# Optimization experiments

Hardware: AMD Instinct MI355X
Metric: run time of the kernel (lower is better)

The kernel has to match this reference:

```python
import jax, jax.numpy as jnp
import numpy as np

B, NPG, DEG = 512, 128, 16          # graphs, nodes/graph, out-degree
N = B * NPG                          # 65536 nodes
E = N * DEG                          # 1048576 edges
IN_DIM, HID, HEADS = 11, 32, 4
K1 = int(np.ceil(0.8 * NPG))         # 103 nodes/graph after pool1
K2 = int(np.ceil(0.8 * K1))          # 83 nodes/graph after pool2


def gat_conv(x, src, dst, mask, W, a_s, a_d, b, n_nodes):
    # PyG GATConv (concat=True, add_self_loops=True, eval mode -> no dropout)
    xp = (x @ W).reshape(n_nodes, HEADS, HID)            # [N,H,C]
    as_ = jnp.einsum('nhc,hc->nh', xp, a_s)
    ad_ = jnp.einsum('nhc,hc->nh', xp, a_d)
    loop = jnp.arange(n_nodes)
    s = jnp.concatenate([src, loop])
    d = jnp.concatenate([dst, loop])
    m = jnp.concatenate([mask, jnp.ones(n_nodes, bool)])
    logit = jax.nn.leaky_relu(as_[s] + ad_[d], 0.2)      # [E+N,H]
    logit = jnp.where(m[:, None], logit, -1e9)
    mx = jax.ops.segment_max(logit, d, num_segments=n_nodes)
    ex = jnp.exp(logit - mx[d]) * m[:, None]
    den = jax.ops.segment_sum(ex, d, num_segments=n_nodes)
    alpha = ex / (den[d] + 1e-16)                        # segment softmax over dst
    out = jax.ops.segment_sum(alpha[:, :, None] * xp[s], d, num_segments=n_nodes)
    return out.reshape(n_nodes, HEADS * HID) + b


def topk_pool(x, src, dst, mask, w, npg, k):
    # PyG TopKPooling: score = tanh((x*w).sum(-1)/||w||); keep top ceil(ratio*n) per graph
    nb = x.shape[0] // npg
    score = jnp.tanh((x @ w) / jnp.linalg.norm(w))
    vals, idx = jax.lax.top_k(score.reshape(nb, npg), k)  # [B,k]
    perm = (idx + (jnp.arange(nb) * npg)[:, None]).reshape(-1)
    x_new = x[perm] * vals.reshape(-1, 1)
    remap = jnp.full(nb * npg, -1).at[perm].set(jnp.arange(nb * k))
    ns, nd = remap[src], remap[dst]
    m = mask & (ns >= 0) & (nd >= 0)
    return x_new, jnp.where(m, ns, 0), jnp.where(m, nd, 0), m


def setup_inputs():
    key = jax.random.key(0)
    ks = jax.random.split(key, 24)
    s = 0.05
    x = jax.random.normal(ks[0], (N, IN_DIM), jnp.float32)
    src = jnp.repeat(jnp.arange(N), DEG)
    dst = (src // NPG) * NPG + jax.random.randint(ks[1], (E,), 0, NPG)
    edge_index = jnp.stack([src, dst])
    edge_attr = jax.random.normal(ks[2], (E, 4), jnp.float32)
    batch = jnp.repeat(jnp.arange(B), NPG)
    p = dict(
        W_g1=jax.random.normal(ks[3], (IN_DIM, HEADS * HID), jnp.float32) * s,
        att_src1=jax.random.normal(ks[4], (HEADS, HID), jnp.float32) * s,
        att_dst1=jax.random.normal(ks[5], (HEADS, HID), jnp.float32) * s,
        b_g1=jnp.zeros((HEADS * HID,), jnp.float32),
        W_t1=jax.random.normal(ks[6], (HEADS * HID, HID), jnp.float32) * s,
        b_t1=jnp.zeros((HID,), jnp.float32),
        pool_w1=jax.random.normal(ks[7], (HID,), jnp.float32) * s,
        W_g2=jax.random.normal(ks[8], (HID, HEADS * HID), jnp.float32) * s,
        att_src2=jax.random.normal(ks[9], (HEADS, HID), jnp.float32) * s,
        att_dst2=jax.random.normal(ks[10], (HEADS, HID), jnp.float32) * s,
        b_g2=jnp.zeros((HEADS * HID,), jnp.float32),
        W_t2=jax.random.normal(ks[11], (HEADS * HID, HID), jnp.float32) * s,
        b_t2=jnp.zeros((HID,), jnp.float32),
        pool_w2=jax.random.normal(ks[12], (HID,), jnp.float32) * s,
        W_l1=jax.random.normal(ks[13], (2 * HID, 256), jnp.float32) * s,
        b_l1=jnp.zeros((256,), jnp.float32),
        W_l2=jax.random.normal(ks[14], (256, 1024), jnp.float32) * s,
        b_l2=jnp.zeros((1024,), jnp.float32),
        W_l3=jax.random.normal(ks[15], (1024, 1), jnp.float32) * s,
        b_l3=jnp.zeros((1,), jnp.float32),
    )
    return dict(x=x, edge_index=edge_index, edge_attr=edge_attr, batch=batch, **p)


def reference(x, edge_index, edge_attr, batch,
              W_g1, att_src1, att_dst1, b_g1, W_t1, b_t1, pool_w1,
              W_g2, att_src2, att_dst2, b_g2, W_t2, b_t2, pool_w2,
              W_l1, b_l1, W_l2, b_l2, W_l3, b_l3):
    # edge_attr is ignored (GATConv built without edge_dim); batch is implicit
    # in the fixed equal-size graph layout.  Eval mode -> dropout disabled.
    src, dst = edge_index[0], edge_index[1]
    mask = jnp.ones(E, bool)
    h = jax.nn.relu(gat_conv(x, src, dst, mask, W_g1, att_src1, att_dst1, b_g1, N))
    h = h @ W_t1 + b_t1
    h, src, dst, mask = topk_pool(h, src, dst, mask, pool_w1, NPG, K1)
    h1 = h.reshape(B, K1, HID)
    g1 = jnp.concatenate([h1.max(1), h1.mean(1)], axis=1)   # [B, 2*HID]
    h = jax.nn.relu(gat_conv(h, src, dst, mask, W_g2, att_src2, att_dst2, b_g2, B * K1))
    h = h @ W_t2 + b_t2
    h, src, dst, mask = topk_pool(h, src, dst, mask, pool_w2, K1, K2)
    h2 = h.reshape(B, K2, HID)
    g2 = jnp.concatenate([h2.max(1), h2.mean(1)], axis=1)
    g = g1 + g2
    g = jax.nn.relu(g @ W_l1 + b_l1)
    g = jax.nn.relu(g @ W_l2 + b_l2)
    return g @ W_l3 + b_l3                                   # [B,1]
```

## Files before the change

kernel.cpp:

```cpp
#include <hip/hip_runtime.h>
#include <math.h>

constexpr int NPGc  = 128;
constexpr int NG    = 512;
constexpr int EPGc  = 2048;
constexpr int ETOT  = 1048576;
constexpr int IND   = 11;
constexpr int HIDc  = 32;
constexpr int FD    = 128;
constexpr int K1c   = 103;
constexpr int K2c   = 83;
constexpr int NN    = NG * NPGc;
constexpr int N2c   = NG * K1c;
constexpr int EPAD  = 2432;
constexpr int SBCAP = 2560;
constexpr int OFFSTR= 264;

__device__ __forceinline__ float lrelu(float x){ return fmaxf(x, 0.2f*x); }

__device__ __forceinline__ void agg4(const float4* __restrict__ X4, int r, int cbase, float e,
                                     float4& A0, float4& A1, float4& A2, float4& A3)
{
    int b = r * 8, s = r & 7;
    float4 u0 = X4[b + ((cbase+0) ^ s)];
    A0.x = fmaf(e, u0.x, A0.x); A0.y = fmaf(e, u0.y, A0.y); A0.z = fmaf(e, u0.z, A0.z); A0.w = fmaf(e, u0.w, A0.w);
    float4 u1 = X4[b + ((cbase+1) ^ s)];
    A1.x = fmaf(e, u1.x, A1.x); A1.y = fmaf(e, u1.y, A1.y); A1.z = fmaf(e, u1.z, A1.z); A1.w = fmaf(e, u1.w, A1.w);
    float4 u2 = X4[b + ((cbase+2) ^ s)];
    A2.x = fmaf(e, u2.x, A2.x); A2.y = fmaf(e, u2.y, A2.y); A2.z = fmaf(e, u2.z, A2.z); A2.w = fmaf(e, u2.w, A2.w);
    float4 u3 = X4[b + ((cbase+3) ^ s)];
    A3.x = fmaf(e, u3.x, A3.x); A3.y = fmaf(e, u3.y, A3.y); A3.z = fmaf(e, u3.z, A3.z); A3.w = fmaf(e, u3.w, A3.w);
}

template<int KIN>
__device__ void foldDev(const float* __restrict__ Wg, const float* __restrict__ avs,
                        const float* __restrict__ avd, float* __restrict__ S, float* __restrict__ D, int t)
{
    if (t < KIN * 4) {
        int k = t >> 2, h = t & 3;
        float s = 0.f, d = 0.f;
        for (int j = 0; j < HIDc; j++) {
            float w = Wg[k*FD + h*HIDc + j];
            s = fmaf(w, avs[h*HIDc + j], s);
            d = fmaf(w, avd[h*HIDc + j], d);
        }
        S[t] = s; D[t] = d;
    }
}

__global__ __launch_bounds__(256) void k_prep(const int* __restrict__ ei,
    const float* __restrict__ W1g, const float* __restrict__ s1, const float* __restrict__ d1,
    const float* __restrict__ W2g, const float* __restrict__ s2, const float* __restrict__ d2,
    int* __restrict__ csrOff, unsigned char* __restrict__ csrSB,
    float* __restrict__ S1, float* __restrict__ D1, float* __restrict__ S2, float* __restrict__ D2)
{
    int b = blockIdx.x, t = threadIdx.x;
    if (b >= NG) {
        if (b == NG)     foldDev<IND>(W1g, s1, d1, S1, D1, t);
        else             foldDev<HIDc>(W2g, s2, d2, S2, D2, t);
        return;
    }
    int g = b;
    __shared__ int cnt[128], cur[128], offL[129];
    __shared__ __align__(16) unsigned char sbL[SBCAP];
    const int FILL1 = (int)0x80808080u;
    if (t < 128) cnt[t] = 0;
    if (t < SBCAP/16) ((int4*)sbL)[t] = make_int4(FILL1, FILL1, FILL1, FILL1);
    __syncthreads();
    const int* dstG = ei + ETOT + g * EPGc;
    int dnv[8];
    #pragma unroll
    for (int q = 0; q < 8; q++) {
        int e = t + 256*q;
        dnv[q] = dstG[e] - g * NPGc;
        atomicAdd(&cnt[dnv[q]], 1);
    }
    __syncthreads();
    if (t < 64) {
        int c0 = cnt[2*t], c1 = cnt[2*t + 1];
        int p0 = (c0 + 3) & ~3, p1 = (c1 + 3) & ~3;
        int ps = p0 + p1, P = ps;
        #pragma unroll
        for (int dl = 1; dl < 64; dl <<= 1) { int v = __shfl_up(P, dl); if (t >= dl) P += v; }
        int E0 = P - ps;
        offL[2*t] = E0; offL[2*t + 1] = E0 + p0;
        cur[2*t]  = E0; cur[2*t + 1]  = E0 + p0;
        if (t == 63) offL[128] = P;
    }
    __syncthreads();
    #pragma unroll
    for (int q = 0; q < 8; q++) {
        int e = t + 256*q;
        int pos = atomicAdd(&cur[dnv[q]], 1);
        sbL[pos] = (unsigned char)(e >> 4);
    }
    __syncthreads();
    if (t < SBCAP/16) ((int4*)(csrSB + (size_t)g * SBCAP))[t] = ((const int4*)sbL)[t];
    if (t <= 128) csrOff[g*OFFSTR + t] = offL[t];
    if (t < 128)  csrOff[g*OFFSTR + 132 + t] = cur[t];
}

template<int NNODE, int KIN>
__global__ __launch_bounds__(256) void k_gat(
    const float* __restrict__ xin, const float* __restrict__ Wg,
    const float* __restrict__ WsS, const float* __restrict__ WsD,
    const int* __restrict__ csrOff, const unsigned char* __restrict__ csrSB,
    const float* __restrict__ bias, const float* __restrict__ Wt,
    float* __restrict__ htp)
{
    int g = blockIdx.x, h = blockIdx.y, t = threadIdx.x;
    __shared__ __align__(16) float xpL[NNODE * 32];
    __shared__ __align__(16) float WL[KIN * 32];
    __shared__ __align__(16) unsigned char sbL[SBCAP];
    __shared__ float asL[NNODE + 1], adL[NNODE];
    __shared__ unsigned short offL[NNODE + 1];

    const float* xg = xin + (size_t)g * NNODE * KIN;

    for (int i = t; i < KIN * 32; i += 256) { int k = i >> 5, c = i & 31; WL[i] = Wg[k*FD + h*32 + c]; }
    if (t <= NNODE) offL[t] = (unsigned short)csrOff[g*OFFSTR + t];
    if (t < SBCAP/16) ((int4*)sbL)[t] = ((const int4*)(csrSB + (size_t)g * SBCAP))[t];
    if (t == 0) asL[NNODE] = -1e30f;
    __syncthreads();

    for (int p = t; p < NNODE * 8; p += 256) {
        int n = p >> 3, c4 = p & 7;
        float4 acc = make_float4(0.f, 0.f, 0.f, 0.f);
        if constexpr ((KIN & 3) == 0) {
            const float4* xr4 = (const float4*)(xg + (size_t)n * KIN);
            #pragma unroll
            for (int k4 = 0; k4 < KIN/4; k4++) {
                float4 xv = xr4[k4];
                float4 w;
                w = *(const float4*)&WL[(k4*4+0)*32 + c4*4];
                acc.x = fmaf(xv.x, w.x, acc.x); acc.y = fmaf(xv.x, w.y, acc.y); acc.z = fmaf(xv.x, w.z, acc.z); acc.w = fmaf(xv.x, w.w, acc.w);
                w = *(const float4*)&WL[(k4*4+1)*32 + c4*4];
                acc.x = fmaf(xv.y, w.x, acc.x); acc.y = fmaf(xv.y, w.y, acc.y); acc.z = fmaf(xv.y, w.z, acc.z); acc.w = fmaf(xv.y, w.w, acc.w);
                w = *(const float4*)&WL[(k4*4+2)*32 + c4*4];
                acc.x = fmaf(xv.z, w.x, acc.x); acc.y = fmaf(xv.z, w.y, acc.y); acc.z = fmaf(xv.z, w.z, acc.z); acc.w = fmaf(xv.z, w.w, acc.w);
                w = *(const float4*)&WL[(k4*4+3)*32 + c4*4];
                acc.x = fmaf(xv.w, w.x, acc.x); acc.y = fmaf(xv.w, w.y, acc.y); acc.z = fmaf(xv.w, w.z, acc.z); acc.w = fmaf(xv.w, w.w, acc.w);
            }
        } else {
            const float* xr = xg + (size_t)n * KIN;
            #pragma unroll
            for (int k = 0; k < KIN; k++) {
                float xv = xr[k];
                float4 w4 = *(const float4*)&WL[k*32 + c4*4];
                acc.x = fmaf(xv, w4.x, acc.x); acc.y = fmaf(xv, w4.y, acc.y);
                acc.z = fmaf(xv, w4.z, acc.z); acc.w = fmaf(xv, w4.w, acc.w);
            }
        }
        ((float4*)xpL)[n*8 + (c4 ^ (n & 7))] = acc;
    }
    if (t < NNODE) {
        const float* xr = xg + (size_t)t * KIN;
        float s = 0.f, d = 0.f;
        #pragma unroll
        for (int k = 0; k < KIN; k++) { float v = xr[k]; s = fmaf(v, WsS[k*4 + h], s); d = fmaf(v, WsD[k*4 + h], d); }
        asL[t] = s; adL[t] = d;
    }
    __syncthreads();

    const float4* X4 = (const float4*)xpL;
    float4 A0, A1, A2, A3;
    int n = 0, cbase = 0;
    bool act = (t < NNODE * 2);
    if (act) {
        n = t >> 1;
        const int half = t & 1;
        cbase = half * 4;
        float as_n = asL[n], adn = adL[n];
        int lo = offL[n], hi = offL[n + 1];
        int mid = lo + (((hi - lo) >> 3) << 2);
        int slo = half ? mid : lo;
        int shi = half ? hi  : mid;
        float mx = -INFINITY;
        for (int i = slo; i < shi; i += 4) {
            unsigned int q4 = *(const unsigned int*)(sbL + i);
            float a0 = asL[q4 & 255], a1 = asL[(q4 >> 8) & 255];
            float a2 = asL[(q4 >> 16) & 255], a3 = asL[q4 >> 24];
            mx = fmaxf(fmaxf(fmaxf(fmaxf(mx, a0), a1), a2), a3);
        }
        mx = fmaxf(mx, __shfl_xor(mx, 1));
        mx = fmaxf(mx, as_n);
        float m = lrelu(mx + adn);
        float den = half ? 0.f : expf(lrelu(as_n + adn) - m);
        for (int i = slo; i < shi; i += 4) {
            unsigned int q4 = *(const unsigned int*)(sbL + i);
            den += expf(lrelu(asL[q4 & 255] + adn) - m);
            den += expf(lrelu(asL[(q4 >> 8) & 255] + adn) - m);
            den += expf(lrelu(asL[(q4 >> 16) & 255] + adn) - m);
            den += expf(lrelu(asL[q4 >> 24] + adn) - m);
        }
        den += __shfl_xor(den, 1);
        float inv = 1.f / (den + 1e-16f);
        float w0 = expf(lrelu(as_n + adn) - m);
        int sw = n & 7, nb = n * 8;
        float4 v0 = X4[nb + ((cbase+0) ^ sw)];
        A0 = make_float4(w0*v0.x, w0*v0.y, w0*v0.z, w0*v0.w);
        float4 v1 = X4[nb + ((cbase+1) ^ sw)];
        A1 = make_float4(w0*v1.x, w0*v1.y, w0*v1.z, w0*v1.w);
        float4 v2 = X4[nb + ((cbase+2) ^ sw)];
        A2 = make_float4(w0*v2.x, w0*v2.y, w0*v2.z, w0*v2.w);
        float4 v3 = X4[nb + ((cbase+3) ^ sw)];
        A3 = make_float4(w0*v3.x, w0*v3.y, w0*v3.z, w0*v3.w);
        for (int s = lo; s < hi; s += 4) {
            unsigned int q4 = *(const unsigned int*)(sbL + s);
            int s0 = q4 & 255, s1 = (q4 >> 8) & 255, s2 = (q4 >> 16) & 255, s3 = q4 >> 24;
            float e0 = expf(lrelu(asL[s0] + adn) - m);
            float e1 = expf(lrelu(asL[s1] + adn) - m);
            float e2 = expf(lrelu(asL[s2] + adn) - m);
            float e3 = expf(lrelu(asL[s3] + adn) - m);
            agg4(X4, min(s0, NNODE-1), cbase, e0, A0, A1, A2, A3);
            agg4(X4, min(s1, NNODE-1), cbase, e1, A0, A1, A2, A3);
            agg4(X4, min(s2, NNODE-1), cbase, e2, A0, A1, A2, A3);
            agg4(X4, min(s3, NNODE-1), cbase, e3, A0, A1, A2, A3);
        }
        const float* bb = bias + h*32 + cbase*4;
        float4 b0 = *(const float4*)(bb);
        float4 b1 = *(const float4*)(bb + 4);
        float4 b2 = *(const float4*)(bb + 8);
        float4 b3 = *(const float4*)(bb + 12);
        A0.x = fmaxf(fmaf(A0.x, inv, b0.x), 0.f); A0.y = fmaxf(fmaf(A0.y, inv, b0.y), 0.f);
        A0.z = fmaxf(fmaf(A0.z, inv, b0.z), 0.f); A0.w = fmaxf(fmaf(A0.w, inv, b0.w), 0.f);
        A1.x = fmaxf(fmaf(A1.x, inv, b1.x), 0.f); A1.y = fmaxf(fmaf(A1.y, inv, b1.y), 0.f);
        A1.z = fmaxf(fmaf(A1.z, inv, b1.z), 0.f); A1.w = fmaxf(fmaf(A1.w, inv, b1.w), 0.f);
        A2.x = fmaxf(fmaf(A2.x, inv, b2.x), 0.f); A2.y = fmaxf(fmaf(A2.y, inv, b2.y), 0.f);
        A2.z = fmaxf(fmaf(A2.z, inv, b2.z), 0.f); A2.w = fmaxf(fmaf(A2.w, inv, b2.w), 0.f);
        A3.x = fmaxf(fmaf(A3.x, inv, b3.x), 0.f); A3.y = fmaxf(fmaf(A3.y, inv, b3.y), 0.f);
        A3.z = fmaxf(fmaf(A3.z, inv, b3.z), 0.f); A3.w = fmaxf(fmaf(A3.w, inv, b3.w), 0.f);
    }
    __syncthreads();
    if (act) {
        float4* X4w = (float4*)xpL;
        int sw = n & 7, nb = n * 8;
        X4w[nb + ((cbase+0) ^ sw)] = A0;
        X4w[nb + ((cbase+1) ^ sw)] = A1;
        X4w[nb + ((cbase+2) ^ sw)] = A2;
        X4w[nb + ((cbase+3) ^ sw)] = A3;
    }
    __syncthreads();

    {
        const int n0 = t >> 3, j4 = t & 7;
        const float* WtH = Wt + h*1024 + j4*4;
        #pragma unroll
        for (int rr = 0; rr < 4; rr++) {
            int nn = n0 + rr*32;
            if (nn < NNODE) {
                float4 acc = make_float4(0.f, 0.f, 0.f, 0.f);
                int sw = nn & 7, nb = nn * 8;
                #pragma unroll
                for (int c4 = 0; c4 < 8; c4++) {
                    float4 xv = X4[nb + (c4 ^ sw)];
                    float4 w;
                    w = *(const float4*)(WtH + (c4*4+0)*32);
                    acc.x = fmaf(xv.x, w.x, acc.x); acc.y = fmaf(xv.x, w.y, acc.y); acc.z = fmaf(xv.x, w.z, acc.z); acc.w = fmaf(xv.x, w.w, acc.w);
                    w = *(const float4*)(WtH + (c4*4+1)*32);
                    acc.x = fmaf(xv.y, w.x, acc.x); acc.y = fmaf(xv.y, w.y, acc.y); acc.z = fmaf(xv.y, w.z, acc.z); acc.w = fmaf(xv.y, w.w, acc.w);
                    w = *(const float4*)(WtH + (c4*4+2)*32);
                    acc.x = fmaf(xv.z, w.x, acc.x); acc.y = fmaf(xv.z, w.y, acc.y); acc.z = fmaf(xv.z, w.z, acc.z); acc.w = fmaf(xv.z, w.w, acc.w);
                    w = *(const float4*)(WtH + (c4*4+3)*32);
                    acc.x = fmaf(xv.w, w.x, acc.x); acc.y = fmaf(xv.w, w.y, acc.y); acc.z = fmaf(xv.w, w.z, acc.z); acc.w = fmaf(xv.w, w.w, acc.w);
                }
                *(float4*)(htp + ((size_t)(g * NNODE + nn) * 4 + h) * 32 + j4 * 4) = acc;
            }
        }
    }
}

template<int NIN, int KEEP, bool FIRST>
__global__ __launch_bounds__(512) void k_linpool(
    const float* __restrict__ htp, const float* __restrict__ bt, const float* __restrict__ pw,
    float* __restrict__ xnew, const int* __restrict__ ei,
    int* __restrict__ csrOffW, unsigned char* __restrict__ sbW,
    float* __restrict__ gfeat, const float* __restrict__ gprev,
    const float* __restrict__ W1, const float* __restrict__ b1,
    const float* __restrict__ W2, const float* __restrict__ b2,
    const float* __restrict__ W3, const float* __restrict__ b3,
    float* __restrict__ outp)
{
    int g = blockIdx.x, t = threadIdx.x;
    __shared__ float htL[NIN * 33];
    __shared__ float scoreL[NIN];
    __shared__ int rnkL[NIN];
    __shared__ int cnt[128], cur[128], offL[129];
    __shared__ __align__(16) unsigned char sbL[SBCAP];
    __shared__ float gvec[64];
    __shared__ float h1L[256], red[512];

    for (int p = t; p < NIN * 8; p += 512) {
        int n = p >> 3, q = p & 7;
        const float4* row = (const float4*)(htp + (size_t)(g * NIN + n) * 128);
        float4 s = ((const float4*)bt)[q];
        float4 p0 = row[q], p1 = row[8 + q], p2 = row[16 + q], p3 = row[24 + q];
        s.x += p0.x; s.y += p0.y; s.z += p0.z; s.w += p0.w;
        s.x += p1.x; s.y += p1.y; s.z += p1.z; s.w += p1.w;
        s.x += p2.x; s.y += p2.y; s.z += p2.z; s.w += p2.w;
        s.x += p3.x; s.y += p3.y; s.z += p3.z; s.w += p3.w;
        float* d = htL + n*33 + q*4;
        d[0] = s.x; d[1] = s.y; d[2] = s.z; d[3] = s.w;
    }
    __syncthreads();

    float nrm; { float ss = 0.f; for (int k = 0; k < HIDc; k++) { float w = pw[k]; ss = fmaf(w, w, ss); } nrm = sqrtf(ss); }
    if (t < NIN) {
        float dot = 0.f;
        #pragma unroll
        for (int k = 0; k < HIDc; k++) dot = fmaf(htL[t*33 + k], pw[k], dot);
        scoreL[t] = tanhf(dot / nrm);
    }
    __syncthreads();
    if (t < NIN) {
        float si = scoreL[t]; int rank = 0;
        #pragma unroll 8
        for (int q = 0; q < NIN; q++) {
            float sj = scoreL[q];
            rank += (sj > si || (sj == si && q < t)) ? 1 : 0;
        }
        rnkL[t] = (rank < KEEP) ? rank : -1;
    }
    __syncthreads();
    if constexpr (FIRST) {
        for (int p = t; p < NIN * 32; p += 512) {
            int n = p >> 5, jj = p & 31;
            int rk = rnkL[n];
            if (rk >= 0) xnew[((size_t)g*KEEP + rk)*HIDc + jj] = htL[n*33 + jj] * scoreL[n];
        }
    }
    if (t < HIDc) {
        float mx = -INFINITY, sm = 0.f;
        #pragma unroll 4
        for (int n = 0; n < NIN; n++) {
            if (rnkL[n] >= 0) { float v = htL[n*33 + t] * scoreL[n]; mx = fmaxf(mx, v); sm += v; }
        }
        float mean = sm / (float)KEEP;
        if constexpr (FIRST) {
            gfeat[(size_t)g*64 + t]      = mx;
            gfeat[(size_t)g*64 + 32 + t] = mean;
        } else {
            gvec[t]      = gprev[(size_t)g*64 + t] + mx;
            gvec[32 + t] = gprev[(size_t)g*64 + 32 + t] + mean;
        }
    }

    if constexpr (FIRST) {
        __syncthreads();
        const int FILL2 = (int)0x67676767u;
        if (t < 128) cnt[t] = 0;
        if (t < SBCAP/16) ((int4*)sbL)[t] = make_int4(FILL2, FILL2, FILL2, FILL2);
        __syncthreads();
        const int* dstG = ei + ETOT + g * EPGc;
        int snv[4], dnv[4];
        #pragma unroll
        for (int q = 0; q < 4; q++) {
            int e = t + 512*q;
            int s = rnkL[e >> 4], d = rnkL[dstG[e] - g * NPGc];
            bool ok = (s >= 0 && d >= 0);
            snv[q] = s; dnv[q] = ok ? d : -1;
            if (ok) atomicAdd(&cnt[d], 1);
        }
        __syncthreads();
        if (t < 64) {
            int c0 = cnt[2*t], c1 = cnt[2*t + 1];
            int p0 = (c0 + 3) & ~3, p1 = (c1 + 3) & ~3;
            int ps = p0 + p1, P = ps;
            #pragma unroll
            for (int dl = 1; dl < 64; dl <<= 1) { int v = __shfl_up(P, dl); if (t >= dl) P += v; }
            int E0 = P - ps;
            offL[2*t] = E0; offL[2*t + 1] = E0 + p0;
            cur[2*t]  = E0; cur[2*t + 1]  = E0 + p0;
            if (t == 63) offL[128] = P;
        }
        __syncthreads();
        #pragma unroll
        for (int q = 0; q < 4; q++) {
            if (dnv[q] >= 0) {
                int pos = atomicAdd(&cur[dnv[q]], 1);
                sbL[pos] = (unsigned char)snv[q];
            }
        }
        __syncthreads();
        if (t < SBCAP/16) ((int4*)(sbW + (size_t)g * SBCAP))[t] = ((const int4*)sbL)[t];
        if (t <= K1c) csrOffW[g*OFFSTR + t] = offL[t];
        if (t < K1c)  csrOffW[g*OFFSTR + 132 + t] = cur[t];
    } else {
        __syncthreads();
        if (t < 256) {
            float a = b1[t];
            #pragma unroll 8
            for (int k = 0; k < 64; k++) a = fmaf(gvec[k], W1[k*256 + t], a);
            h1L[t] = fmaxf(a, 0.f);
        }
        __syncthreads();
        float2 bq = *(const float2*)(b2 + 2*t);
        float c0 = bq.x, c1 = bq.y;
        const float2* w2r = (const float2*)W2 + t;
        #pragma unroll 8
        for (int i = 0; i < 256; i++) {
            float hv = h1L[i];
            float2 w = w2r[(size_t)i * 512];
            c0 = fmaf(hv, w.x, c0);
            c1 = fmaf(hv, w.y, c1);
        }
        float2 w3q = *(const float2*)(W3 + 2*t);
        float p = fmaf(fmaxf(c0, 0.f), w3q.x, fmaxf(c1, 0.f) * w3q.y);
        red[t] = p;
        __syncthreads();
        for (int s = 256; s > 0; s >>= 1) { if (t < s) red[t] += red[t + s]; __syncthreads(); }
        if (t == 0) outp[g] = red[0] + b3[0];
    }
}

extern "C" void kernel_launch(void* const* d_in, const int* in_sizes, int n_in,
                              void* d_out, int out_size, void* d_ws, size_t ws_size,
                              hipStream_t stream)
{
    const float* x    = (const float*)d_in[0];
    const int*   ei   = (const int*)  d_in[1];
    const float* W_g1 = (const float*)d_in[4];
    const float* as1w = (const float*)d_in[5];
    const float* ad1w = (const float*)d_in[6];
    const float* b_g1 = (const float*)d_in[7];
    const float* W_t1 = (const float*)d_in[8];
    const float* b_t1 = (const float*)d_in[9];
    const float* pw1  = (const float*)d_in[10];
    const float* W_g2 = (const float*)d_in[11];
    const float* as2w = (const float*)d_in[12];
    const float* ad2w = (const float*)d_in[13];
    const float* b_g2 = (const float*)d_in[14];
    const float* W_t2 = (const float*)d_in[15];
    const float* b_t2 = (const float*)d_in[16];
    const float* pw2  = (const float*)d_in[17];
    const float* W_l1 = (const float*)d_in[18];
    const float* b_l1 = (const float*)d_in[19];
    const float* W_l2 = (const float*)d_in[20];
    const float* b_l2 = (const float*)d_in[21];
    const float* W_l3 = (const float*)d_in[22];
    const float* b_l3 = (const float*)d_in[23];
    float* out = (float*)d_out;

    char* ws = (char*)d_ws;
    size_t off = 0;
    auto alloc = [&](size_t bytes) -> void* {
        void* p = (void*)(ws + off);
        off += ((bytes + 255) / 256) * 256;
        return p;
    };
    float* htp1  = (float*)alloc((size_t)NN * 128 * 4);
    float* htp2  = (float*)alloc((size_t)N2c * 128 * 4);
    float* x2    = (float*)alloc((size_t)N2c * HIDc * 4);
    float* g1    = (float*)alloc((size_t)NG * 64 * 4);
    float* wsS1  = (float*)alloc(64 * 4);
    float* wsD1  = (float*)alloc(64 * 4);
    float* wsS2  = (float*)alloc(128 * 4);
    float* wsD2  = (float*)alloc(128 * 4);
    int*   off1  = (int*)  alloc((size_t)NG * OFFSTR * 4);
    unsigned char* sb1 = (unsigned char*)alloc((size_t)NG * SBCAP);
    int*   off2  = (int*)  alloc((size_t)NG * OFFSTR * 4);
    unsigned char* sb2 = (unsigned char*)alloc((size_t)NG * SBCAP);

    k_prep<<<NG + 2, 256, 0, stream>>>(ei, W_g1, as1w, ad1w, W_g2, as2w, ad2w,
                                       off1, sb1, wsS1, wsD1, wsS2, wsD2);

    k_gat<NPGc, IND><<<dim3(NG, 4), 256, 0, stream>>>(
        x, W_g1, wsS1, wsD1, off1, sb1, b_g1, W_t1, htp1);

    k_linpool<NPGc, K1c, true><<<NG, 512, 0, stream>>>(
        htp1, b_t1, pw1, x2, ei, off2, sb2, g1, nullptr,
        nullptr, nullptr, nullptr, nullptr, nullptr, nullptr, nullptr);

    k_gat<K1c, HIDc><<<dim3(NG, 4), 256, 0, stream>>>(
        x2, W_g2, wsS2, wsD2, off2, sb2, b_g2, W_t2, htp2);

    k_linpool<K1c, K2c, false><<<NG, 512, 0, stream>>>(
        htp2, b_t2, pw2, nullptr, nullptr, nullptr, nullptr, nullptr, g1,
        W_l1, b_l1, W_l2, b_l2, W_l3, b_l3, out);
}
```

Baseline: 284.6 us.

## Process two graphs per block in linpool kernels to reuse MLP weights

```diff
diff --git a/kernel.cpp b/kernel.cpp
--- a/kernel.cpp
+++ b/kernel.cpp
@@ -281,135 +281,158 @@
     const float* __restrict__ W3, const float* __restrict__ b3,
     float* __restrict__ outp)
 {
-    int g = blockIdx.x, t = threadIdx.x;
-    __shared__ float htL[NIN * 33];
-    __shared__ float scoreL[NIN];
-    __shared__ int rnkL[NIN];
-    __shared__ int cnt[128], cur[128], offL[129];
-    __shared__ __align__(16) unsigned char sbL[SBCAP];
-    __shared__ float gvec[64];
-    __shared__ float h1L[256], red[512];
-
-    for (int p = t; p < NIN * 8; p += 512) {
-        int n = p >> 3, q = p & 7;
-        const float4* row = (const float4*)(htp + (size_t)(g * NIN + n) * 128);
+    const int t = threadIdx.x;
+    const int gg = t >> 8, tl = t & 255;
+    const int g0 = blockIdx.x * 2;
+    __shared__ float htL[2][NIN * 33];
+    __shared__ float scoreL[2][NIN];
+    __shared__ int rnkL[2][NIN];
+    __shared__ int cnt[2][128], cur[2][128], offL[2][129];
+    __shared__ __align__(16) unsigned char sbL[2][SBCAP];
+    __shared__ float gvec[2][64];
+    __shared__ float h1L[2][256];
+    __shared__ float red[2][512];
+
+    for (int p = t; p < 2 * NIN * 8; p += 512) {
+        int g2 = p / (NIN * 8), rem = p - g2 * (NIN * 8);
+        int n = rem >> 3, q = rem & 7;
+        const float4* row = (const float4*)(htp + (size_t)((g0 + g2) * NIN + n) * 128);
         float4 s = ((const float4*)bt)[q];
         float4 p0 = row[q], p1 = row[8 + q], p2 = row[16 + q], p3 = row[24 + q];
         s.x += p0.x; s.y += p0.y; s.z += p0.z; s.w += p0.w;
         s.x += p1.x; s.y += p1.y; s.z += p1.z; s.w += p1.w;
         s.x += p2.x; s.y += p2.y; s.z += p2.z; s.w += p2.w;
         s.x += p3.x; s.y += p3.y; s.z += p3.z; s.w += p3.w;
-        float* d = htL + n*33 + q*4;
+        float* d = htL[g2] + n*33 + q*4;
         d[0] = s.x; d[1] = s.y; d[2] = s.z; d[3] = s.w;
     }
     __syncthreads();
 
     float nrm; { float ss = 0.f; for (int k = 0; k < HIDc; k++) { float w = pw[k]; ss = fmaf(w, w, ss); } nrm = sqrtf(ss); }
-    if (t < NIN) {
+    if (tl < NIN) {
         float dot = 0.f;
         #pragma unroll
-        for (int k = 0; k < HIDc; k++) dot = fmaf(htL[t*33 + k], pw[k], dot);
-        scoreL[t] = tanhf(dot / nrm);
-    }
-    __syncthreads();
-    if (t < NIN) {
-        float si = scoreL[t]; int rank = 0;
+        for (int k = 0; k < HIDc; k++) dot = fmaf(htL[gg][tl*33 + k], pw[k], dot);
+        scoreL[gg][tl] = tanhf(dot / nrm);
+    }
+    __syncthreads();
+    if (tl < NIN) {
+        float si = scoreL[gg][tl]; int rank = 0;
         #pragma unroll 8
         for (int q = 0; q < NIN; q++) {
-            float sj = scoreL[q];
-            rank += (sj > si || (sj == si && q < t)) ? 1 : 0;
-        }
-        rnkL[t] = (rank < KEEP) ? rank : -1;
+            float sj = scoreL[gg][q];
+            rank += (sj > si || (sj == si && q < tl)) ? 1 : 0;
+        }
+        rnkL[gg][tl] = (rank < KEEP) ? rank : -1;
     }
     __syncthreads();
     if constexpr (FIRST) {
-        for (int p = t; p < NIN * 32; p += 512) {
-            int n = p >> 5, jj = p & 31;
-            int rk = rnkL[n];
-            if (rk >= 0) xnew[((size_t)g*KEEP + rk)*HIDc + jj] = htL[n*33 + jj] * scoreL[n];
-        }
-    }
-    if (t < HIDc) {
+        for (int p = t; p < 2 * NIN * 32; p += 512) {
+            int g2 = p / (NIN * 32), rem = p - g2 * (NIN * 32);
+            int n = rem >> 5, jj = rem & 31;
+            int rk = rnkL[g2][n];
+            if (rk >= 0) xnew[((size_t)(g0 + g2)*KEEP + rk)*HIDc + jj] = htL[g2][n*33 + jj] * scoreL[g2][n];
+        }
+    }
+    if (tl < HIDc) {
         float mx = -INFINITY, sm = 0.f;
         #pragma unroll 4
         for (int n = 0; n < NIN; n++) {
-            if (rnkL[n] >= 0) { float v = htL[n*33 + t] * scoreL[n]; mx = fmaxf(mx, v); sm += v; }
+            if (rnkL[gg][n] >= 0) { float v = htL[gg][n*33 + tl] * scoreL[gg][n]; mx = fmaxf(mx, v); sm += v; }
         }
         float mean = sm / (float)KEEP;
         if constexpr (FIRST) {
-            gfeat[(size_t)g*64 + t]      = mx;
-            gfeat[(size_t)g*64 + 32 + t] = mean;
+            gfeat[(size_t)(g0 + gg)*64 + tl]      = mx;
+            gfeat[(size_t)(g0 + gg)*64 + 32 + tl] = mean;
         } else {
-            gvec[t]      = gprev[(size_t)g*64 + t] + mx;
-            gvec[32 + t] = gprev[(size_t)g*64 + 32 + t] + mean;
+            gvec[gg][tl]      = gprev[(size_t)(g0 + gg)*64 + tl] + mx;
+            gvec[gg][32 + tl] = gprev[(size_t)(g0 + gg)*64 + 32 + tl] + mean;
         }
     }
 
     if constexpr (FIRST) {
         __syncthreads();
         const int FILL2 = (int)0x67676767u;
-        if (t < 128) cnt[t] = 0;
-        if (t < SBCAP/16) ((int4*)sbL)[t] = make_int4(FILL2, FILL2, FILL2, FILL2);
-        __syncthreads();
-        const int* dstG = ei + ETOT + g * EPGc;
-        int snv[4], dnv[4];
+        if (t < 256) cnt[t >> 7][t & 127] = 0;
+        if (t < 2*(SBCAP/16)) {
+            int g2 = t / (SBCAP/16), idx = t - g2*(SBCAP/16);
+            ((int4*)sbL[g2])[idx] = make_int4(FILL2, FILL2, FILL2, FILL2);
+        }
+        __syncthreads();
+        const int* dstG = ei + ETOT + (g0 + gg) * EPGc;
+        int snv[8], dnv[8];
         #pragma unroll
-        for (int q = 0; q < 4; q++) {
-            int e = t + 512*q;
-            int s = rnkL[e >> 4], d = rnkL[dstG[e] - g * NPGc];
+        for (int q = 0; q < 8; q++) {
+            int e = tl + 256*q;
+            int s = rnkL[gg][e >> 4], d = rnkL[gg][dstG[e] - (g0 + gg) * NPGc];
             bool ok = (s >= 0 && d >= 0);
             snv[q] = s; dnv[q] = ok ? d : -1;
-            if (ok) atomicAdd(&cnt[d], 1);
-        }
-        __syncthreads();
-        if (t < 64) {
-            int c0 = cnt[2*t], c1 = cnt[2*t + 1];
+            if (ok) atomicAdd(&cnt[gg][d], 1);
+        }
+        __syncthreads();
+        if (t < 128) {
+            int sg = t >> 6, lane = t & 63;
+            int c0 = cnt[sg][2*lane], c1 = cnt[sg][2*lane + 1];
             int p0 = (c0 + 3) & ~3, p1 = (c1 + 3) & ~3;
             int ps = p0 + p1, P = ps;
             #pragma unroll
-            for (int dl = 1; dl < 64; dl <<= 1) { int v = __shfl_up(P, dl); if (t >= dl) P += v; }
+            for (int dl = 1; dl < 64; dl <<= 1) { int v = __shfl_up(P, dl); if (lane >= dl) P += v; }
             int E0 = P - ps;
-            offL[2*t] = E0; offL[2*t + 1] = E0 + p0;
-            cur[2*t]  = E0; cur[2*t + 1]  = E0 + p0;
-            if (t == 63) offL[128] = P;
+            offL[sg][2*lane] = E0; offL[sg][2*lane + 1] = E0 + p0;
+            cur[sg][2*lane]  = E0; cur[sg][2*lane + 1]  = E0 + p0;
+            if (lane == 63) offL[sg][128] = P;
         }
         __syncthreads();
         #pragma unroll
-        for (int q = 0; q < 4; q++) {
+        for (int q = 0; q < 8; q++) {
             if (dnv[q] >= 0) {
-                int pos = atomicAdd(&cur[dnv[q]], 1);
-                sbL[pos] = (unsigned char)snv[q];
+                int pos = atomicAdd(&cur[gg][dnv[q]], 1);
+                sbL[gg][pos] = (unsigned char)snv[q];
             }
         }
         __syncthreads();
-        if (t < SBCAP/16) ((int4*)(sbW + (size_t)g * SBCAP))[t] = ((const int4*)sbL)[t];
-        if (t <= K1c) csrOffW[g*OFFSTR + t] = offL[t];
-        if (t < K1c)  csrOffW[g*OFFSTR + 132 + t] = cur[t];
+        if (t < 2*(SBCAP/16)) {
+            int g2 = t / (SBCAP/16), idx = t - g2*(SBCAP/16);
+            ((int4*)(sbW + (size_t)(g0 + g2) * SBCAP))[idx] = ((const int4*)sbL[g2])[idx];
+        }
+        if (tl <= K1c) csrOffW[(g0 + gg)*OFFSTR + tl] = offL[gg][tl];
+        if (tl < K1c)  csrOffW[(g0 + gg)*OFFSTR + 132 + tl] = cur[gg][tl];
     } else {
         __syncthreads();
         if (t < 256) {
-            float a = b1[t];
+            float a0 = b1[t], a1v = b1[t];
             #pragma unroll 8
-            for (int k = 0; k < 64; k++) a = fmaf(gvec[k], W1[k*256 + t], a);
-            h1L[t] = fmaxf(a, 0.f);
+            for (int k = 0; k < 64; k++) {
+                float w = W1[k*256 + t];
+                a0  = fmaf(gvec[0][k], w, a0);
+                a1v = fmaf(gvec[1][k], w, a1v);
+            }
+            h1L[0][t] = fmaxf(a0, 0.f);
+            h1L[1][t] = fmaxf(a1v, 0.f);
         }
         __syncthreads();
         float2 bq = *(const float2*)(b2 + 2*t);
-        float c0 = bq.x, c1 = bq.y;
+        float c00 = bq.x, c01 = bq.y;
+        float c10 = bq.x, c11 = bq.y;
         const float2* w2r = (const float2*)W2 + t;
         #pragma unroll 8
         for (int i = 0; i < 256; i++) {
-            float hv = h1L[i];
             float2 w = w2r[(size_t)i * 512];
-            c0 = fmaf(hv, w.x, c0);
-            c1 = fmaf(hv, w.y, c1);
+            float hv0 = h1L[0][i], hv1 = h1L[1][i];
+            c00 = fmaf(hv0, w.x, c00);
+            c01 = fmaf(hv0, w.y, c01);
+            c10 = fmaf(hv1, w.x, c10);
+            c11 = fmaf(hv1, w.y, c11);
         }
         float2 w3q = *(const float2*)(W3 + 2*t);
-        float p = fmaf(fmaxf(c0, 0.f), w3q.x, fmaxf(c1, 0.f) * w3q.y);
-        red[t] = p;
-        __syncthreads();
-        for (int s = 256; s > 0; s >>= 1) { if (t < s) red[t] += red[t + s]; __syncthreads(); }
-        if (t == 0) outp[g] = red[0] + b3[0];
+        red[0][t] = fmaf(fmaxf(c00, 0.f), w3q.x, fmaxf(c01, 0.f) * w3q.y);
+        red[1][t] = fmaf(fmaxf(c10, 0.f), w3q.x, fmaxf(c11, 0.f) * w3q.y);
+        __syncthreads();
+        for (int s = 256; s > 0; s >>= 1) {
+            if (t < s) { red[0][t] += red[0][t + s]; red[1][t] += red[1][t + s]; }
+            __syncthreads();
+        }
+        if (t == 0) { outp[g0] = red[0][0] + b3[0]; outp[g0 + 1] = red[1][0] + b3[0]; }
     }
 }
 
@@ -467,14 +490,14 @@
     k_gat<NPGc, IND><<<dim3(NG, 4), 256, 0, stream>>>(
         x, W_g1, wsS1, wsD1, off1, sb1, b_g1, W_t1, htp1);
 
-    k_linpool<NPGc, K1c, true><<<NG, 512, 0, stream>>>(
+    k_linpool<NPGc, K1c, true><<<NG/2, 512, 0, stream>>>(
         htp1, b_t1, pw1, x2, ei, off2, sb2, g1, nullptr,
         nullptr, nullptr, nullptr, nullptr, nullptr, nullptr, nullptr);
 
     k_gat<K1c, HIDc><<<dim3(NG, 4), 256, 0, stream>>>(
         x2, W_g2, wsS2, wsD2, off2, sb2, b_g2, W_t2, htp2);
 
-    k_linpool<K1c, K2c, false><<<NG, 512, 0, stream>>>(
+    k_linpool<K1c, K2c, false><<<NG/2, 512, 0, stream>>>(
         htp2, b_t2, pw2, nullptr, nullptr, nullptr, nullptr, nullptr, g1,
         W_l1, b_l1, W_l2, b_l2, W_l3, b_l3, out);
 }
```

After: 274.8 us. 1.04x faster.
